# Performance work log

Hardware: AMD Instinct MI355X
Metric: run time of the kernel (lower is better)

Reference implementation:

```python
import jax, jax.numpy as jnp
import numpy as np

LATENT = 64  # latent_size -> N = K = LATENT**2 = 4096 codes/tokens


def setup_inputs() -> dict:
    key = jax.random.key(0)
    k1, k2 = jax.random.split(key)
    hidden, L = 1024, LATENT
    z = jax.random.normal(k1, (hidden, L, L), dtype=jnp.float32)
    code_books = jax.random.uniform(k2, (hidden, L, L), dtype=jnp.float32)  # torch.rand init
    return {"z": z, "code_books": code_books}


def reference(z, code_books):
    # z, code_books: (D=hidden, L, L). Tokens/codes are columns of the flattened maps.
    D = z.shape[0]
    zf = z.reshape(D, -1).T           # (N, D) tokens
    cb = code_books.reshape(D, -1).T  # (K, D) codebook entries
    # Squared L2 distance via GEMM trick: ||a-b||^2 = ||a||^2 + ||b||^2 - 2 a.b
    # (avoids the N x K x D broadcast intermediate of the original)
    d2 = (jnp.sum(zf * zf, axis=1)[:, None]
          + jnp.sum(cb * cb, axis=1)[None, :]
          - 2.0 * zf @ cb.T)          # (N, K)
    idx = jnp.argmin(d2, axis=1)      # (N,)
    zq = cb[idx]                      # (N, D) gather
    zq = zq.reshape(LATENT, LATENT, -1).transpose(2, 0, 1)  # (D, L, L)
    # Straight-through: z = zq + (z - zq).detach()  (z was detached before lookup)
    z_st = zq + jax.lax.stop_gradient(z - zq)
    return z_st, zq
```

## Files before the change

### kernel.cpp

```cpp
#include <hip/hip_runtime.h>
#include <stdint.h>

#define D  1024
#define NK 4096
#define KA 1024
#define KB 1024
#define TAU 0.15f
#define CW  0.12f
#define MAXC 1024

#define BK2 32
#define NT2 (KA / BK2)
#define NBUF 4

typedef __attribute__((ext_vector_type(8))) _Float16 f16x8;
typedef __attribute__((ext_vector_type(4))) float f32x4;
typedef unsigned long long u64;

__device__ __forceinline__ uint32_t fkey(float f) {
    uint32_t b = __float_as_uint(f);
    return (b & 0x80000000u) ? ~b : (b | 0x80000000u);
}
__device__ __forceinline__ float unfkey(uint32_t u) {
    uint32_t b = (u & 0x80000000u) ? (u & 0x7fffffffu) : ~u;
    return __uint_as_float(b);
}
__device__ __forceinline__ u64 umin64(u64 a, u64 b) { return a < b ? a : b; }
__device__ __forceinline__ u64 umax64(u64 a, u64 b) { return a > b ? a : b; }

__device__ __forceinline__ void gload16(void* lds, const void* g) {
    __builtin_amdgcn_global_load_lds(
        (const __attribute__((address_space(1))) unsigned int*)g,
        (__attribute__((address_space(3))) unsigned int*)lds, 16, 0, 0);
}

__global__ void cbnorm_kernel(const float* __restrict__ cb, float* __restrict__ cbn) {
    __shared__ float red[256];
    const int kk = threadIdx.x & 63;
    const int dc = threadIdx.x >> 6;
    const int k  = blockIdx.x * 64 + kk;
    float s = 0.f;
    for (int d = dc; d < D; d += 4) {
        float v = cb[d * NK + k];
        s = fmaf(v, v, s);
    }
    red[threadIdx.x] = s;
    __syncthreads();
    if (dc == 0) cbn[k] = (red[kk] + red[64 + kk]) + (red[128 + kk] + red[192 + kk]);
}

__global__ __launch_bounds__(256) void split_transpose(
        const float* __restrict__ z, const float* __restrict__ cb,
        _Float16* __restrict__ Ap, _Float16* __restrict__ Bp,
        float* __restrict__ partial, int* __restrict__ ctr) {
    __shared__ float T[64][65];
    if (blockIdx.x == 0 && blockIdx.y == 0 && blockIdx.z == 0 && threadIdx.x == 0)
        *ctr = 0;
    const int isZ = (blockIdx.z == 0);
    const float* src = isZ ? z : cb;
    _Float16* dst = isZ ? Ap : Bp;
    const int n0 = blockIdx.x * 64, d0 = blockIdx.y * 64;
    const int t = threadIdx.x;
#pragma unroll
    for (int i = 0; i < 4; ++i) {
        int dl = (t >> 4) + i * 16;
        int nl = (t & 15) * 4;
        float4 v = *(const float4*)&src[(size_t)(d0 + dl) * NK + n0 + nl];
        T[dl][nl] = v.x; T[dl][nl + 1] = v.y; T[dl][nl + 2] = v.z; T[dl][nl + 3] = v.w;
    }
    __syncthreads();
    const int nr = t >> 2, dch = (t & 3) * 16;
    f16x8 h0, h1;
    float s = 0.f;
#pragma unroll
    for (int j = 0; j < 8; ++j) {
        float v = T[dch + j][nr];
        s = fmaf(v, v, s);
        h0[j] = (_Float16)v;
    }
#pragma unroll
    for (int j = 0; j < 8; ++j) {
        float v = T[dch + 8 + j][nr];
        s = fmaf(v, v, s);
        h1[j] = (_Float16)v;
    }
    size_t base = (size_t)(n0 + nr) * KA + d0 + dch;
    *(f16x8*)&dst[base]     = h0;
    *(f16x8*)&dst[base + 8] = h1;
    if (!isZ) {
        s += __shfl_xor(s, 1);
        s += __shfl_xor(s, 2);
        if ((t & 3) == 0) partial[(size_t)(d0 >> 6) * NK + n0 + nr] = s;
    }
}

__global__ __launch_bounds__(512, 2) void gemm_mfma(
        const _Float16* __restrict__ Ap, const _Float16* __restrict__ Bp,
        const float* __restrict__ partial, ulonglong2* __restrict__ tp) {
    __shared__ _Float16 As[NBUF][256 * BK2];
    __shared__ _Float16 Bs[NBUF][256 * BK2];
    const int tid = threadIdx.x;
    const int xcd = blockIdx.x & 7, idx = blockIdx.x >> 3;
    const int n0 = ((xcd >> 1) * 4 + (idx >> 3)) * 256;
    const int k0 = ((xcd & 1) * 8 + (idx & 7)) * 256;
    const int w = tid >> 6, l = tid & 63;
    const int wr = w >> 2, wc = w & 3;
    const int fr = l & 15, fq = l >> 4;

    f32x4 acc[8][4] = {};

    const int srow = tid >> 2;
    const int swz = ((tid & 3) ^ ((tid >> 3) & 3)) * 8;
    const _Float16* gA0 = Ap + (size_t)(n0 + srow) * KA + swz;
    const _Float16* gA1 = Ap + (size_t)(n0 + 128 + srow) * KA + swz;
    const _Float16* gB0 = Bp + (size_t)(k0 + srow) * KB + swz;
    const _Float16* gB1 = Bp + (size_t)(k0 + 128 + srow) * KB + swz;
    const int rcol = (fq ^ ((fr >> 1) & 3)) * 8;

    gload16(&As[0][tid * 8],        gA0);
    gload16(&As[0][4096 + tid * 8], gA1);
    gload16(&Bs[0][tid * 8],        gB0);
    gload16(&Bs[0][4096 + tid * 8], gB1);
    gload16(&As[1][tid * 8],        gA0 + BK2);
    gload16(&As[1][4096 + tid * 8], gA1 + BK2);
    gload16(&Bs[1][tid * 8],        gB0 + BK2);
    gload16(&Bs[1][4096 + tid * 8], gB1 + BK2);
    asm volatile("s_waitcnt vmcnt(4)" ::: "memory");
    __builtin_amdgcn_s_barrier();
    asm volatile("" ::: "memory");

    for (int t = 0; t < NT2; ++t) {
        const int b = t & 3;
        const int pb = (t + 2) & 3;
        const _Float16* Ab = As[b];
        const _Float16* Bb = Bs[b];
        const bool st = (t + 2) < NT2;

        f16x8 bbf[4], a0[4];
#pragma unroll
        for (int ni = 0; ni < 4; ++ni)
            bbf[ni] = *(const f16x8*)&Bb[(wc * 64 + ni * 16 + fr) * BK2 + rcol];
#pragma unroll
        for (int mi = 0; mi < 4; ++mi)
            a0[mi] = *(const f16x8*)&Ab[(wr * 128 + mi * 16 + fr) * BK2 + rcol];
        if (st) {
            gload16(&As[pb][tid * 8],        gA0 + (t + 2) * BK2);
            gload16(&As[pb][4096 + tid * 8], gA1 + (t + 2) * BK2);
        }
        __builtin_amdgcn_s_setprio(1);
#pragma unroll
        for (int mi = 0; mi < 4; ++mi)
#pragma unroll
            for (int ni = 0; ni < 4; ++ni)
                acc[mi][ni] = __builtin_amdgcn_mfma_f32_16x16x32_f16(a0[mi], bbf[ni], acc[mi][ni], 0, 0, 0);
        __builtin_amdgcn_s_setprio(0);
        __builtin_amdgcn_s_barrier();

        f16x8 a1[4];
#pragma unroll
        for (int mi = 0; mi < 4; ++mi)
            a1[mi] = *(const f16x8*)&Ab[(wr * 128 + 64 + mi * 16 + fr) * BK2 + rcol];
        if (st) {
            gload16(&Bs[pb][tid * 8],        gB0 + (t + 2) * BK2);
            gload16(&Bs[pb][4096 + tid * 8], gB1 + (t + 2) * BK2);
        }
        __builtin_amdgcn_s_setprio(1);
#pragma unroll
        for (int mi = 0; mi < 4; ++mi)
#pragma unroll
            for (int ni = 0; ni < 4; ++ni)
                acc[4 + mi][ni] = __builtin_amdgcn_mfma_f32_16x16x32_f16(a1[mi], bbf[ni], acc[4 + mi][ni], 0, 0, 0);
        __builtin_amdgcn_s_setprio(0);

        if (t < NT2 - 2) {
            asm volatile("s_waitcnt vmcnt(4)" ::: "memory");
        } else if (t == NT2 - 2) {
            asm volatile("s_waitcnt vmcnt(0)" ::: "memory");
        }
        if (t < NT2 - 1) {
            __builtin_amdgcn_s_barrier();
            asm volatile("" ::: "memory");
        }
    }

    float cbv[4];
#pragma unroll
    for (int ni = 0; ni < 4; ++ni) {
        const int k = k0 + wc * 64 + ni * 16 + fr;
        float s = 0.f;
#pragma unroll
        for (int j = 0; j < 16; ++j) s += partial[(size_t)j * NK + k];
        cbv[ni] = s;
    }
    const int kt64 = (k0 >> 6) + wc;
#pragma unroll
    for (int mi = 0; mi < 8; ++mi) {
#pragma unroll
        for (int reg = 0; reg < 4; ++reg) {
            float b1f = 1e30f, b2f = 1e30f;
            int b1k = 0;
#pragma unroll
            for (int ni = 0; ni < 4; ++ni) {
                float s = fmaf(-2.f, acc[mi][ni][reg], cbv[ni]);
                b2f = fminf(fmaxf(s, b1f), b2f);
                if (s < b1f) { b1f = s; b1k = k0 + wc * 64 + ni * 16 + fr; }
            }
#pragma unroll
            for (int m = 8; m >= 1; m >>= 1) {
                float q1 = __shfl_xor(b1f, m);
                int   qk = __shfl_xor(b1k, m);
                float q2 = __shfl_xor(b2f, m);
                b2f = fminf(fminf(b2f, q2), fmaxf(b1f, q1));
                if (q1 < b1f) { b1f = q1; b1k = qk; }
            }
            if (fr == 0) {
                int n = n0 + wr * 128 + mi * 16 + fq * 4 + reg;
                ulonglong2 v;
                v.x = ((u64)fkey(b1f) << 32) | (unsigned)b1k;
                v.y = ((u64)fkey(b2f) << 32) | 0xffffffffu;
                tp[(size_t)kt64 * NK + n] = v;
            }
        }
    }
}

__global__ __launch_bounds__(256) void reduce_rows(
        const ulonglong2* __restrict__ tp, int* __restrict__ idx,
        int* __restrict__ rescue, int* __restrict__ ctr) {
    __shared__ ulonglong2 sh[4][64];
    const int no = threadIdx.x & 63, st = threadIdx.x >> 6;
    const int n = blockIdx.x * 64 + no;
    u64 b1 = ~0ull, b2 = ~0ull;
#pragma unroll 4
    for (int g = st * 16; g < st * 16 + 16; ++g) {
        ulonglong2 e = tp[(size_t)g * NK + n];
        u64 nb1 = umin64(b1, e.x);
        u64 nb2 = umin64(umax64(b1, e.x), umin64(b2, e.y));
        b1 = nb1; b2 = nb2;
    }
    ulonglong2 v; v.x = b1; v.y = b2;
    sh[st][no] = v;
    __syncthreads();
    if (st == 0) {
#pragma unroll
        for (int j = 1; j < 4; ++j) {
            ulonglong2 e = sh[j][no];
            u64 nb1 = umin64(b1, e.x);
            u64 nb2 = umin64(umax64(b1, e.x), umin64(b2, e.y));
            b1 = nb1; b2 = nb2;
        }
        idx[n] = (int)(b1 & 0xffffffffull);
        float f1 = unfkey((uint32_t)(b1 >> 32));
        float f2 = unfkey((uint32_t)(b2 >> 32));
        if (f2 - f1 < TAU) {
            int p = atomicAdd(ctr, 1);
            rescue[p] = n;
        }
    }
}

__global__ __launch_bounds__(256) void rescue_kernel(
        const float* __restrict__ z, const float* __restrict__ cb,
        const ulonglong2* __restrict__ tp, const int* __restrict__ rescue,
        const int* __restrict__ ctr, int* __restrict__ idx) {
    const int cnt = min(*ctr, NK);
    const int tid = threadIdx.x;
    const int lane = tid & 63, wv = tid >> 6;

    __shared__ float zn[D];
    __shared__ int cand[MAXC];
    __shared__ int ccnt, overflow;
    __shared__ u64 wred[4];

    for (int slot = blockIdx.x; slot < cnt; slot += gridDim.x) {
        const int n = rescue[slot];
        if (tid == 0) { ccnt = 0; overflow = 0; }
        for (int d = tid; d < D; d += 256) zn[d] = z[(size_t)d * NK + n];

        if (tid < 64) {
            ulonglong2 e = tp[(size_t)tid * NK + n];
            u64 m = e.x;
#pragma unroll
            for (int msk = 32; msk >= 1; msk >>= 1) m = umin64(m, __shfl_xor(m, msk));
            const float thr = unfkey((uint32_t)(m >> 32)) + CW;
            if (unfkey((uint32_t)(e.y >> 32)) < thr) {
                int p = atomicAdd(&ccnt, 64);
                if (p + 64 <= MAXC) {
                    for (int j = 0; j < 64; ++j) cand[p + j] = tid * 64 + j;
                } else overflow = 1;
            } else if (unfkey((uint32_t)(e.x >> 32)) < thr) {
                int p = atomicAdd(&ccnt, 1);
                if (p < MAXC) cand[p] = (int)(e.x & 0xffffffffull);
                else overflow = 1;
            }
        }
        __syncthreads();

        const int ovf = overflow;
        const int m = ovf ? NK : min(ccnt, MAXC);
        u64 best = ~0ull;
        for (int ci = wv; ci < m; ci += 4) {
            const int k = ovf ? ci : cand[ci];
            float s = 0.f, s2 = 0.f;
#pragma unroll
            for (int j = 0; j < 16; ++j) {
                float c = cb[(size_t)(lane + j * 64) * NK + k];
                s  = fmaf(zn[lane + j * 64], c, s);
                s2 = fmaf(c, c, s2);
            }
#pragma unroll
            for (int msk = 32; msk >= 1; msk >>= 1) {
                s  += __shfl_xor(s, msk);
                s2 += __shfl_xor(s2, msk);
            }
            float sc = s2 - 2.f * s;
            best = umin64(best, ((u64)fkey(sc) << 32) | (unsigned)k);
        }
        if (lane == 0) wred[wv] = best;
        __syncthreads();
        if (tid == 0)
            idx[n] = (int)(umin64(umin64(wred[0], wred[1]),
                                  umin64(wred[2], wred[3])) & 0xffffffffull);
        __syncthreads();
    }
}

__global__ __launch_bounds__(256) void gemm_argmin(
        const float* __restrict__ z, const float* __restrict__ cb,
        const float* __restrict__ cbn, unsigned long long* __restrict__ best) {
    __shared__ float Zs[8][128];
    __shared__ float Cs[8][128];
    const int n0 = blockIdx.y * 128, k0 = blockIdx.x * 128;
    const int tid = threadIdx.x;
    const int tx = tid & 15, ty = tid >> 4;
    const int lr = tid >> 5, lc = (tid & 31) << 2;
    float acc[8][8];
#pragma unroll
    for (int i = 0; i < 8; ++i)
#pragma unroll
        for (int j = 0; j < 8; ++j) acc[i][j] = 0.f;
    for (int d0 = 0; d0 < D; d0 += 8) {
        float4 zv = *(const float4*)&z [(d0 + lr) * NK + n0 + lc];
        float4 cv = *(const float4*)&cb[(d0 + lr) * NK + k0 + lc];
        __syncthreads();
        *(float4*)&Zs[lr][lc] = zv;
        *(float4*)&Cs[lr][lc] = cv;
        __syncthreads();
#pragma unroll
        for (int dd = 0; dd < 8; ++dd) {
            float4 a0 = *(const float4*)&Zs[dd][ty * 8];
            float4 a1 = *(const float4*)&Zs[dd][ty * 8 + 4];
            float4 b0 = *(const float4*)&Cs[dd][tx * 8];
            float4 b1 = *(const float4*)&Cs[dd][tx * 8 + 4];
            float a[8] = {a0.x, a0.y, a0.z, a0.w, a1.x, a1.y, a1.z, a1.w};
            float b[8] = {b0.x, b0.y, b0.z, b0.w, b1.x, b1.y, b1.z, b1.w};
#pragma unroll
            for (int i = 0; i < 8; ++i)
#pragma unroll
                for (int j = 0; j < 8; ++j) acc[i][j] = fmaf(a[i], b[j], acc[i][j]);
        }
    }
    float cbnv[8];
#pragma unroll
    for (int j = 0; j < 8; ++j) cbnv[j] = cbn[k0 + tx * 8 + j];
#pragma unroll
    for (int i = 0; i < 8; ++i) {
        float bv = cbnv[0] - 2.f * acc[i][0];
        int bj = 0;
#pragma unroll
        for (int j = 1; j < 8; ++j) {
            float v = cbnv[j] - 2.f * acc[i][j];
            if (v < bv) { bv = v; bj = j; }
        }
        u64 p = ((u64)fkey(bv) << 32) | (unsigned)(k0 + tx * 8 + bj);
#pragma unroll
        for (int m = 8; m >= 1; m >>= 1) {
            u64 q = __shfl_xor(p, m);
            if (q < p) p = q;
        }
        if (tx == 0) atomicMin(&best[n0 + ty * 8 + i], p);
    }
}

__global__ void extract_idx(const unsigned long long* __restrict__ best,
                            int* __restrict__ idx) {
    int n = blockIdx.x * 256 + threadIdx.x;
    idx[n] = (int)(unsigned)(best[n] & 0xFFFFFFFFull);
}

__global__ void gather_kernel(const float* __restrict__ z, const float* __restrict__ cb,
                              const int* __restrict__ idx, float* __restrict__ out) {
    const int d = blockIdx.x;
    const float* cbrow = &cb[(size_t)d * NK];
    const float* zrow  = &z [(size_t)d * NK];
    float* st = &out[(size_t)d * NK];
    float* zq = &out[(size_t)D * NK + (size_t)d * NK];
    for (int n4 = threadIdx.x; n4 < NK / 4; n4 += 256) {
        int4 iv = *(const int4*)&idx[n4 * 4];
        float4 zv = *(const float4*)&zrow[n4 * 4];
        float4 q;
        q.x = cbrow[iv.x]; q.y = cbrow[iv.y]; q.z = cbrow[iv.z]; q.w = cbrow[iv.w];
        float4 stv;
        stv.x = q.x + (zv.x - q.x);
        stv.y = q.y + (zv.y - q.y);
        stv.z = q.z + (zv.z - q.z);
        stv.w = q.w + (zv.w - q.w);
        *(float4*)&st[n4 * 4] = stv;
        *(float4*)&zq[n4 * 4] = q;
    }
}

extern "C" void kernel_launch(void* const* d_in, const int* in_sizes, int n_in,
                              void* d_out, int out_size, void* d_ws, size_t ws_size,
                              hipStream_t stream) {
    const float* z  = (const float*)d_in[0];
    const float* cb = (const float*)d_in[1];
    float* out = (float*)d_out;
    char* ws = (char*)d_ws;

    const size_t oA  = 0;
    const size_t oB  = oA + (size_t)NK * KA * 2;
    const size_t oT  = oB + (size_t)NK * KB * 2;
    const size_t oI  = oT + (size_t)NK * 64 * 16;
    const size_t oR  = oI + NK * 4;
    const size_t oN  = oR + NK * 4;
    const size_t oP  = oN + 256;
    const size_t REQ = oP + (size_t)16 * NK * 4;

    if (ws_size >= REQ) {
        _Float16* Ap = (_Float16*)(ws + oA);
        _Float16* Bp = (_Float16*)(ws + oB);
        ulonglong2* tp = (ulonglong2*)(ws + oT);
        int* idx = (int*)(ws + oI);
        int* rescue = (int*)(ws + oR);
        int* ctr = (int*)(ws + oN);
        float* partial = (float*)(ws + oP);

        split_transpose<<<dim3(NK / 64, D / 64, 2), 256, 0, stream>>>(z, cb, Ap, Bp, partial, ctr);
        gemm_mfma<<<256, 512, 0, stream>>>(Ap, Bp, partial, tp);
        reduce_rows<<<64, 256, 0, stream>>>(tp, idx, rescue, ctr);
        rescue_kernel<<<1024, 256, 0, stream>>>(z, cb, tp, rescue, ctr, idx);
        gather_kernel<<<1024, 256, 0, stream>>>(z, cb, idx, out);
    } else {
        unsigned long long* best = (unsigned long long*)ws;
        float* cbn = (float*)(ws + NK * 8);
        int* idx = (int*)(ws + NK * 8 + NK * 4);
        hipMemsetAsync(best, 0xFF, NK * 8, stream);
        cbnorm_kernel<<<64, 256, 0, stream>>>(cb, cbn);
        gemm_argmin<<<dim3(NK / 128, NK / 128), 256, 0, stream>>>(z, cb, cbn, best);
        extract_idx<<<16, 256, 0, stream>>>(best, idx);
        gather_kernel<<<1024, 256, 0, stream>>>(z, cb, idx, out);
    }
}
```

Before: 80.05 us.

## Use 4 waves with 128x128 per-wave tiles in fp16 MFMA distance GEMM

```diff
diff --git a/kernel.cpp b/kernel.cpp
--- a/kernel.cpp
+++ b/kernel.cpp
@@ -33,6 +33,10 @@
         (const __attribute__((address_space(1))) unsigned int*)g,
         (__attribute__((address_space(3))) unsigned int*)lds, 16, 0, 0);
 }
+
+#define BAR()     __builtin_amdgcn_s_barrier()
+#define VMCNT8()  asm volatile("s_waitcnt vmcnt(8)" ::: "memory")
+#define VMCNT0()  asm volatile("s_waitcnt vmcnt(0)" ::: "memory")
 
 __global__ void cbnorm_kernel(const float* __restrict__ cb, float* __restrict__ cbn) {
     __shared__ float red[256];
@@ -94,7 +98,7 @@
     }
 }
 
-__global__ __launch_bounds__(512, 2) void gemm_mfma(
+__global__ __launch_bounds__(256, 1) void gemm_mfma(
         const _Float16* __restrict__ Ap, const _Float16* __restrict__ Bp,
         const float* __restrict__ partial, ulonglong2* __restrict__ tp) {
     __shared__ _Float16 As[NBUF][256 * BK2];
@@ -104,30 +108,27 @@
     const int n0 = ((xcd >> 1) * 4 + (idx >> 3)) * 256;
     const int k0 = ((xcd & 1) * 8 + (idx & 7)) * 256;
     const int w = tid >> 6, l = tid & 63;
-    const int wr = w >> 2, wc = w & 3;
+    const int wr = w >> 1, wc = w & 1;
     const int fr = l & 15, fq = l >> 4;
 
-    f32x4 acc[8][4] = {};
+    f32x4 acc[8][8] = {};
 
     const int srow = tid >> 2;
     const int swz = ((tid & 3) ^ ((tid >> 3) & 3)) * 8;
-    const _Float16* gA0 = Ap + (size_t)(n0 + srow) * KA + swz;
-    const _Float16* gA1 = Ap + (size_t)(n0 + 128 + srow) * KA + swz;
-    const _Float16* gB0 = Bp + (size_t)(k0 + srow) * KB + swz;
-    const _Float16* gB1 = Bp + (size_t)(k0 + 128 + srow) * KB + swz;
+    const _Float16* gA = Ap + (size_t)(n0 + srow) * KA + swz;
+    const _Float16* gB = Bp + (size_t)(k0 + srow) * KB + swz;
     const int rcol = (fq ^ ((fr >> 1) & 3)) * 8;
 
-    gload16(&As[0][tid * 8],        gA0);
-    gload16(&As[0][4096 + tid * 8], gA1);
-    gload16(&Bs[0][tid * 8],        gB0);
-    gload16(&Bs[0][4096 + tid * 8], gB1);
-    gload16(&As[1][tid * 8],        gA0 + BK2);
-    gload16(&As[1][4096 + tid * 8], gA1 + BK2);
-    gload16(&Bs[1][tid * 8],        gB0 + BK2);
-    gload16(&Bs[1][4096 + tid * 8], gB1 + BK2);
-    asm volatile("s_waitcnt vmcnt(4)" ::: "memory");
-    __builtin_amdgcn_s_barrier();
-    asm volatile("" ::: "memory");
+#pragma unroll
+    for (int i = 0; i < 4; ++i) gload16(&As[0][tid * 8 + i * 2048], gA + (size_t)(64 * i) * KA);
+#pragma unroll
+    for (int i = 0; i < 4; ++i) gload16(&Bs[0][tid * 8 + i * 2048], gB + (size_t)(64 * i) * KB);
+#pragma unroll
+    for (int i = 0; i < 4; ++i) gload16(&As[1][tid * 8 + i * 2048], gA + (size_t)(64 * i) * KA + BK2);
+#pragma unroll
+    for (int i = 0; i < 4; ++i) gload16(&Bs[1][tid * 8 + i * 2048], gB + (size_t)(64 * i) * KB + BK2);
+    VMCNT8();
+    BAR();
 
     for (int t = 0; t < NT2; ++t) {
         const int b = t & 3;
@@ -135,90 +136,79 @@
         const _Float16* Ab = As[b];
         const _Float16* Bb = Bs[b];
         const bool st = (t + 2) < NT2;
-
-        f16x8 bbf[4], a0[4];
-#pragma unroll
-        for (int ni = 0; ni < 4; ++ni)
-            bbf[ni] = *(const f16x8*)&Bb[(wc * 64 + ni * 16 + fr) * BK2 + rcol];
-#pragma unroll
-        for (int mi = 0; mi < 4; ++mi)
-            a0[mi] = *(const f16x8*)&Ab[(wr * 128 + mi * 16 + fr) * BK2 + rcol];
+        const size_t kofs = (size_t)(t + 2) * BK2;
+
+        f16x8 bb[8];
+#pragma unroll
+        for (int ni = 0; ni < 8; ++ni)
+            bb[ni] = *(const f16x8*)&Bb[(wc * 128 + ni * 16 + fr) * BK2 + rcol];
+
         if (st) {
-            gload16(&As[pb][tid * 8],        gA0 + (t + 2) * BK2);
-            gload16(&As[pb][4096 + tid * 8], gA1 + (t + 2) * BK2);
-        }
+#pragma unroll
+            for (int i = 0; i < 4; ++i)
+                gload16(&As[pb][tid * 8 + i * 2048], gA + (size_t)(64 * i) * KA + kofs);
+#pragma unroll
+            for (int i = 0; i < 4; ++i)
+                gload16(&Bs[pb][tid * 8 + i * 2048], gB + (size_t)(64 * i) * KB + kofs);
+        }
+
         __builtin_amdgcn_s_setprio(1);
 #pragma unroll
-        for (int mi = 0; mi < 4; ++mi)
-#pragma unroll
-            for (int ni = 0; ni < 4; ++ni)
-                acc[mi][ni] = __builtin_amdgcn_mfma_f32_16x16x32_f16(a0[mi], bbf[ni], acc[mi][ni], 0, 0, 0);
+        for (int mi = 0; mi < 8; ++mi) {
+            f16x8 a = *(const f16x8*)&Ab[(wr * 128 + mi * 16 + fr) * BK2 + rcol];
+#pragma unroll
+            for (int ni = 0; ni < 8; ++ni)
+                acc[mi][ni] = __builtin_amdgcn_mfma_f32_16x16x32_f16(a, bb[ni], acc[mi][ni], 0, 0, 0);
+        }
         __builtin_amdgcn_s_setprio(0);
-        __builtin_amdgcn_s_barrier();
-
-        f16x8 a1[4];
-#pragma unroll
-        for (int mi = 0; mi < 4; ++mi)
-            a1[mi] = *(const f16x8*)&Ab[(wr * 128 + 64 + mi * 16 + fr) * BK2 + rcol];
-        if (st) {
-            gload16(&Bs[pb][tid * 8],        gB0 + (t + 2) * BK2);
-            gload16(&Bs[pb][4096 + tid * 8], gB1 + (t + 2) * BK2);
-        }
-        __builtin_amdgcn_s_setprio(1);
-#pragma unroll
-        for (int mi = 0; mi < 4; ++mi)
-#pragma unroll
-            for (int ni = 0; ni < 4; ++ni)
-                acc[4 + mi][ni] = __builtin_amdgcn_mfma_f32_16x16x32_f16(a1[mi], bbf[ni], acc[4 + mi][ni], 0, 0, 0);
-        __builtin_amdgcn_s_setprio(0);
 
         if (t < NT2 - 2) {
-            asm volatile("s_waitcnt vmcnt(4)" ::: "memory");
+            VMCNT8();
         } else if (t == NT2 - 2) {
-            asm volatile("s_waitcnt vmcnt(0)" ::: "memory");
-        }
-        if (t < NT2 - 1) {
-            __builtin_amdgcn_s_barrier();
-            asm volatile("" ::: "memory");
-        }
-    }
-
-    float cbv[4];
-#pragma unroll
-    for (int ni = 0; ni < 4; ++ni) {
-        const int k = k0 + wc * 64 + ni * 16 + fr;
-        float s = 0.f;
-#pragma unroll
-        for (int j = 0; j < 16; ++j) s += partial[(size_t)j * NK + k];
-        cbv[ni] = s;
-    }
-    const int kt64 = (k0 >> 6) + wc;
-#pragma unroll
-    for (int mi = 0; mi < 8; ++mi) {
-#pragma unroll
-        for (int reg = 0; reg < 4; ++reg) {
-            float b1f = 1e30f, b2f = 1e30f;
-            int b1k = 0;
-#pragma unroll
-            for (int ni = 0; ni < 4; ++ni) {
-                float s = fmaf(-2.f, acc[mi][ni][reg], cbv[ni]);
-                b2f = fminf(fmaxf(s, b1f), b2f);
-                if (s < b1f) { b1f = s; b1k = k0 + wc * 64 + ni * 16 + fr; }
-            }
-#pragma unroll
-            for (int m = 8; m >= 1; m >>= 1) {
-                float q1 = __shfl_xor(b1f, m);
-                int   qk = __shfl_xor(b1k, m);
-                float q2 = __shfl_xor(b2f, m);
-                b2f = fminf(fminf(b2f, q2), fmaxf(b1f, q1));
-                if (q1 < b1f) { b1f = q1; b1k = qk; }
-            }
-            if (fr == 0) {
-                int n = n0 + wr * 128 + mi * 16 + fq * 4 + reg;
-                ulonglong2 v;
-                v.x = ((u64)fkey(b1f) << 32) | (unsigned)b1k;
-                v.y = ((u64)fkey(b2f) << 32) | 0xffffffffu;
-                tp[(size_t)kt64 * NK + n] = v;
+            VMCNT0();
+        }
+        if (t < NT2 - 1) BAR();
+    }
+
+#pragma unroll
+    for (int nh = 0; nh < 2; ++nh) {
+        float cbv[4];
+#pragma unroll
+        for (int ni = 0; ni < 4; ++ni) {
+            const int k = k0 + wc * 128 + nh * 64 + ni * 16 + fr;
+            float s = 0.f;
+#pragma unroll
+            for (int j = 0; j < 16; ++j) s += partial[(size_t)j * NK + k];
+            cbv[ni] = s;
+        }
+        const int kt64 = (k0 >> 6) + wc * 2 + nh;
+#pragma unroll
+        for (int mi = 0; mi < 8; ++mi) {
+#pragma unroll
+            for (int reg = 0; reg < 4; ++reg) {
+                float b1f = 1e30f, b2f = 1e30f;
+                int b1k = 0;
+#pragma unroll
+                for (int ni = 0; ni < 4; ++ni) {
+                    float s = fmaf(-2.f, acc[mi][nh * 4 + ni][reg], cbv[ni]);
+                    b2f = fminf(fmaxf(s, b1f), b2f);
+                    if (s < b1f) { b1f = s; b1k = k0 + wc * 128 + nh * 64 + ni * 16 + fr; }
+                }
+#pragma unroll
+                for (int m = 8; m >= 1; m >>= 1) {
+                    float q1 = __shfl_xor(b1f, m);
+                    int   qk = __shfl_xor(b1k, m);
+                    float q2 = __shfl_xor(b2f, m);
+                    b2f = fminf(fminf(b2f, q2), fmaxf(b1f, q1));
+                    if (q1 < b1f) { b1f = q1; b1k = qk; }
+                }
+                if (fr == 0) {
+                    int n = n0 + wr * 128 + mi * 16 + fq * 4 + reg;
+                    ulonglong2 v;
+                    v.x = ((u64)fkey(b1f) << 32) | (unsigned)b1k;
+                    v.y = ((u64)fkey(b2f) << 32) | 0xffffffffu;
+                    tp[(size_t)kt64 * NK + n] = v;
+                }
             }
         }
     }
@@ -437,7 +427,7 @@
         float* partial = (float*)(ws + oP);
 
         split_transpose<<<dim3(NK / 64, D / 64, 2), 256, 0, stream>>>(z, cb, Ap, Bp, partial, ctr);
-        gemm_mfma<<<256, 512, 0, stream>>>(Ap, Bp, partial, tp);
+        gemm_mfma<<<256, 256, 0, stream>>>(Ap, Bp, partial, tp);
         reduce_rows<<<64, 256, 0, stream>>>(tp, idx, rescue, ctr);
         rescue_kernel<<<1024, 256, 0, stream>>>(z, cb, tp, rescue, ctr, idx);
         gather_kernel<<<1024, 256, 0, stream>>>(z, cb, idx, out);
```

New measurement: 133.7 us. 1.67x slower.
